# Optimization experiments

Measured on AMD Instinct MI355X. Metric: run time of the kernel, lower is better.

The kernel has to match this reference:

```python
import jax, jax.numpy as jnp
import numpy as np

EPS = 1e-30


def _logmmexp(P, logW):
    """Stable logsumexp_k(P[..., k] + logW[a, k]) -> (..., a) via max-shifted matmul."""
    mP = jnp.max(P, axis=-1, keepdims=True)          # (..., 1)
    mW = jnp.max(logW, axis=-1, keepdims=True)       # (A, 1)
    out = jnp.einsum('...k,ak->...a', jnp.exp(P - mP), jnp.exp(logW - mW))
    return jnp.log(out) + mP + mW[:, 0]


def _inside_chart(tokens, log_binary, log_lexical):
    B, L = tokens.shape
    N = log_binary.shape[0]
    chart = jnp.full((B, N, L, L + 1), -jnp.inf, dtype=log_lexical.dtype)
    # Base case: chart[:, :, i, i+1] = log_lexical[:, tokens[:, i]]
    lex = jnp.transpose(log_lexical[:, tokens], (1, 0, 2))  # (B, N, L)
    ii = jnp.arange(L)
    chart = chart.at[:, :, ii, ii + 1].set(lex)
    # CKY recursion: loop over span length (structural, static), vectorize over
    # start positions i and split points k.
    for s in range(2, L + 1):
        pos = L - s + 1
        i = np.arange(pos)
        m = np.arange(s - 1)
        k_idx = i[:, None] + m[None, :] + 1                 # (pos, s-1) split points
        left = chart[:, :, i[:, None], k_idx]               # (B, N, pos, s-1)
        right = chart[:, :, k_idx, (i + s)[:, None]]        # (B, N, pos, s-1)
        lt = jnp.transpose(left, (0, 2, 3, 1))              # (B, pos, m, N_B)
        rt = jnp.transpose(right, (0, 2, 3, 1))             # (B, pos, m, N_C)
        # P[b,i,m,B,C] = left + right
        P = lt[..., :, None] + rt[..., None, :]             # (B, pos, m, N, N)
        Pf = P.reshape(B, pos, (s - 1) * N * N)
        logW = jnp.broadcast_to(log_binary[:, None, :, :], (N, s - 1, N, N)).reshape(N, -1)
        scores = _logmmexp(Pf, logW)                        # (B, pos, N_A)
        chart = chart.at[:, :, i, i + s].set(jnp.transpose(scores, (0, 2, 1)))
    return chart


def setup_inputs() -> dict:
    key = jax.random.key(0)
    k1, k2, k3 = jax.random.split(key, 3)
    B, L, N, T = 32, 32, 48, 32000
    tokens = jax.random.randint(k1, (B, L), 0, T)
    binary = jax.random.uniform(k2, (N, N, N), dtype=jnp.float32)
    lexical = jax.random.uniform(k3, (N, T), dtype=jnp.float32)
    return {"tokens": tokens, "binary": binary, "lexical": lexical}


def reference(tokens, binary, lexical):
    start = 0
    log_binary = jnp.log(jnp.clip(binary, EPS))
    log_lexical = jnp.log(jnp.clip(lexical, EPS))
    chart = _inside_chart(tokens, log_binary, log_lexical)
    return chart[:, start, 0, tokens.shape[1]]  # (B,) sentence log-probs
```

## Files before the change

### kernel.cpp

```cpp
#include <hip/hip_runtime.h>
#include <math.h>

#define NNT 48
#define LL 32
#define BB 32
#define N2 2304
#define KSTEPS 72
#define EPSV 1e-30f
#define CH_J ((LL+1)*NNT)
#define SEB_S 2328
#define PD_RS 20
#define PD_T  328
#define PD_W  984
#define NCELL (BB*LL*(LL+1)*NNT)

typedef __attribute__((ext_vector_type(8))) short bf16x8;
typedef __attribute__((ext_vector_type(4))) float f32x4;
typedef __attribute__((ext_vector_type(4))) int   i32x4;

__device__ __forceinline__ int ch_idx(int b, int i, int j, int n) {
    return (((b*LL + i)*(LL+1) + j)*NNT + n);
}
__device__ __forceinline__ unsigned short f2bf(float x) {
    unsigned u = __float_as_uint(x);
    u = (u + 0x7fffu + ((u >> 16) & 1u)) >> 16;
    return (unsigned short)u;
}
__device__ __forceinline__ int cvtpk(float lo, float hi) {
    int r;
    asm("v_cvt_pk_bf16_f32 %0, %1, %2" : "=v"(r) : "v"(lo), "v"(hi));
    return r;
}
__device__ __forceinline__ int uvt_base(int q, int r, int kc) {
    return q*1536 + ((((r << 2) + kc) ^ (r & 7)) << 3);
}
__device__ __forceinline__ float wavemax(float x) {
    #pragma unroll
    for (int o = 32; o; o >>= 1) x = fmaxf(x, __shfl_xor(x, o));
    return x;
}
__device__ __forceinline__ float ch_ld(const float* p) {
    return __hip_atomic_load(p, __ATOMIC_RELAXED, __HIP_MEMORY_SCOPE_AGENT);
}
__device__ __forceinline__ void ch_st(float* p, float v) {
    __hip_atomic_store(p, v, __ATOMIC_RELAXED, __HIP_MEMORY_SCOPE_AGENT);
}
#define LBAR() { asm volatile("s_waitcnt lgkmcnt(0)" ::: "memory"); \
                 __builtin_amdgcn_s_barrier(); }

__global__ void prep_kernel(const float* __restrict__ binary, const int* __restrict__ tokens,
                            const float* __restrict__ lexical, unsigned short* __restrict__ Wp,
                            float* __restrict__ chart, int T) {
    if (blockIdx.x < 432) {
        int idx = blockIdx.x*256 + threadIdx.x;
        int j  = idx & 7;
        int l  = (idx >> 3) & 63;
        int ks = (idx >> 9) % KSTEPS;
        int nt = idx / (KSTEPS*512);
        int e = ks*32 + ((l >> 4) << 3) + j;
        int n = nt*16 + (l & 15);
        int bp = e % 48, c = e / 48;
        Wp[idx] = f2bf(fmaxf(binary[n*N2 + bp*48 + c], EPSV));
    } else if (blockIdx.x < 688) {
        int row = (blockIdx.x - 432)*4 + (threadIdx.x >> 6);
        int lane = threadIdx.x & 63;
        int b = row >> 5, i = row & 31;
        int tok = tokens[b*LL + i];
        float val = (lane < NNT)
            ? __logf(fmaxf(lexical[(size_t)lane*(size_t)T + (size_t)tok], EPSV))
            : -INFINITY;
        float rm = wavemax(val);
        if (lane < NNT) chart[ch_idx(b, i, i+1, lane)] = val;
        if (lane == 0) chart[ch_idx(b, i, 0, i+1)] = rm;
    } else {
        int idx = (blockIdx.x - 688)*256 + threadIdx.x;
        if (idx < NCELL) {
            int n = idx % NNT;
            int r = idx / NNT;
            int j = r % (LL + 1);
            int i = (r / (LL + 1)) % LL;
            if (j != i + 1 && !(j == 0 && n == i + 1))
                chart[idx] = -INFINITY;
        }
    }
}

#define MFMA16(A,B,C) __builtin_amdgcn_mfma_f32_16x16x32_bf16(A,B,C,0,0,0)

#define LDVP(V, C, TCX, VPX)                                                   \
    { _Pragma("unroll")                                                        \
      for (int dt = 0; dt < 8; ++dt) {                                         \
          int t = (C)*8 + dt; int tt = (t < (TCX)) ? t : (TCX) - 1;            \
          int kk = rr + tt*2;                                                  \
          V[dt] = ch_ld((VPX) + kk*CH_J + ln);                                 \
      } }
#define FRESHFIX(V)                                                            \
    { if (freshLDS) {                                                          \
          if (lane == 0) btP = sRm[q + 1][s - 1];                              \
          if (rr == 0) V[0] = sOut[q + 1][ln];                                 \
      } }
#define CONSCH(V, C)                                                           \
    { int pv[4];                                                               \
      _Pragma("unroll")                                                        \
      for (int dp = 0; dp < 4; ++dp) {                                         \
          int t0 = (C)*8 + 2*dp;                                               \
          int tt0 = (t0     < tc) ? t0     : tc - 1;                           \
          int tt1 = (t0 + 1 < tc) ? t0 + 1 : tc - 1;                           \
          float a0 = sRm[q][rr + tt0*2 + 1];                                   \
          float a1 = sRm[q][rr + tt1*2 + 1];                                   \
          float e0 = __expf(V[2*dp]     + a0 - M);                             \
          float e1 = __expf(V[2*dp + 1] + a1 - M);                             \
          pv[dp] = cvtpk(e0, e1);                                              \
      }                                                                        \
      if (lane < NNT) {                                                        \
          int ad = uvt_base(w, lane, (C));                                     \
          *(i32x4*)&sUV[12288 + ad] = (i32x4){pv[0],pv[1],pv[2],pv[3]};        \
      } }

__global__ __launch_bounds__(512, 2) void inside_kernel(
        const unsigned short* __restrict__ Wp,
        float* __restrict__ chart,
        float* __restrict__ out) {
    const int pb = blockIdx.x;
    const int b = pb & 31, c = pb >> 5;
    const int i_base = 28 - 4*c;
    const int tid = threadIdx.x, lane = tid & 63, w = tid >> 6;
    const int fr = lane & 15, kg = lane >> 4;
    const int ln = (lane < NNT) ? lane : 0;
    const int q = w >> 1, rr = w & 1;
    const int i0 = i_base + q;

    __shared__ __align__(16) short sUV[24576];
    __shared__ __align__(16) short sEb[16*SEB_S];
    __shared__ float pD[8*PD_W];
    __shared__ float sRm[4][33];
    __shared__ float sOut[4][NNT];

    for (int x = tid; x < 12288; x += 512) ((int*)sUV)[x] = 0;
    for (int x = tid; x < 18624; x += 512) ((int*)sEb)[x] = 0;
    if (tid < 4)
        sRm[tid][1] = ch_ld(&chart[ch_idx(b, i_base + tid, 0, i_base + tid + 1)]);
    if (w < 4 && lane < NNT)
        sOut[w][lane] = ch_ld(&chart[ch_idx(b, i_base + w, i_base + w + 1, lane)]);

    const bf16x8* wp8 = (const bf16x8*)Wp;
    const int kstart = 9*w;
    bf16x8 wreg[9][3];
    #pragma unroll
    for (int t = 0; t < 9; ++t)
        #pragma unroll
        for (int nt = 0; nt < 3; ++nt)
            wreg[t][nt] = wp8[(nt*KSTEPS + kstart + t)*64 + lane];

    float vvP0[8] = {0,0,0,0,0,0,0,0}, vvP1[8] = {0,0,0,0,0,0,0,0}, btP = 0.f;
    if (i0 <= LL - 2) {
        const int nkn = 1, tcn = (nkn - rr + 1) >> 1;
        if (tcn > 0) {
            const float* vpn = chart + ch_idx(b, i0 + 1, i0 + 2, 0);
            const float* bpn = chart + ch_idx(b, i0 + 1, 0, i0 + 2);
            btP = (lane < nkn) ? ch_ld(bpn + lane*CH_J) : 0.f;
            LDVP(vvP0, 0, tcn, vpn)
        }
    }

    __syncthreads();

    for (int s = 2; s <= LL; ++s) {
        const int nk = s - 1;
        if (i_base > LL - s) return;

        const bool active = (i0 <= LL - s);
        const int tc = active ? ((nk - rr + 1) >> 1) : 0;
        const bool freshLDS = active && (s > 2) && (q < 3);
        float M = -INFINITY;
        f32x4 ea[9];
        #pragma unroll
        for (int z = 0; z < 9; ++z) ea[z] = (f32x4){0.f, 0.f, 0.f, 0.f};

        if (active && rr == ((nk - 1) & 1) && lane < NNT) {
            int tn = (nk - 1 - rr) >> 1;
            float eu = __expf(sOut[q][lane] - sRm[q][s - 1]);
            sUV[uvt_base(w, lane, tn >> 3) + (tn & 7)] = (short)f2bf(eu);
        }

        if (tc > 0) {
            const float* vp = chart + ch_idx(b, i0 + 1, i0 + s, 0);
            const float* bp = chart + ch_idx(b, i0 + 1, 0, i0 + s);

            FRESHFIX(vvP0)
            for (;;) {
                bool bad = (lane < nk) && (btP == -INFINITY);
                #pragma unroll
                for (int dt = 0; dt < 8; ++dt) bad |= (vvP0[dt] == -INFINITY);
                if (tc > 8) {
                    #pragma unroll
                    for (int dt = 0; dt < 8; ++dt) bad |= (vvP1[dt] == -INFINITY);
                }
                if (!__any(bad)) break;
                btP = (lane < nk) ? ch_ld(bp + lane*CH_J) : 0.f;
                LDVP(vvP0, 0, tc, vp)
                if (tc > 8) { LDVP(vvP1, 1, tc, vp) }
                FRESHFIX(vvP0)
            }

            {
                float al = (lane < nk) ? sRm[q][lane + 1] : -INFINITY;
                M = wavemax((lane < nk) ? al + btP : -INFINITY);
            }

            CONSCH(vvP0, 0)
            if (tc > 8) { CONSCH(vvP1, 1) }

            bf16x8 A0 = *(const bf16x8*)&sUV[uvt_base(w,  0 + fr, kg)];
            bf16x8 A1 = *(const bf16x8*)&sUV[uvt_base(w, 16 + fr, kg)];
            bf16x8 A2 = *(const bf16x8*)&sUV[uvt_base(w, 32 + fr, kg)];
            bf16x8 B0 = *(const bf16x8*)&sUV[12288 + uvt_base(w,  0 + fr, kg)];
            bf16x8 B1 = *(const bf16x8*)&sUV[12288 + uvt_base(w, 16 + fr, kg)];
            bf16x8 B2 = *(const bf16x8*)&sUV[12288 + uvt_base(w, 32 + fr, kg)];
            ea[0] = MFMA16(A0,B0,ea[0]); ea[1] = MFMA16(A0,B1,ea[1]); ea[2] = MFMA16(A0,B2,ea[2]);
            ea[3] = MFMA16(A1,B0,ea[3]); ea[4] = MFMA16(A1,B1,ea[4]); ea[5] = MFMA16(A1,B2,ea[5]);
            ea[6] = MFMA16(A2,B0,ea[6]); ea[7] = MFMA16(A2,B1,ea[7]); ea[8] = MFMA16(A2,B2,ea[8]);
        }

        if (s < LL && i0 <= LL - s - 1) {
            const int nkn = s;
            const int tcn = (nkn - rr + 1) >> 1;
            const float* vpn = chart + ch_idx(b, i0 + 1, i0 + s + 1, 0);
            const float* bpn = chart + ch_idx(b, i0 + 1, 0, i0 + s + 1);
            btP = (lane < nkn) ? ch_ld(bpn + lane*CH_J) : 0.f;
            LDVP(vvP0, 0, tcn, vpn)
            if (tcn > 8) { LDVP(vvP1, 1, tcn, vpn) }
        }

        if (active) {
            #pragma unroll
            for (int mt = 0; mt < 3; ++mt) {
                #pragma unroll
                for (int ct = 0; ct < 3; ++ct) {
                    f32x4 d = ea[mt*3 + ct];
                    int e0 = (ct*16 + fr)*48 + mt*16 + kg*4;
                    unsigned lo = (unsigned)cvtpk(d[0], d[1]);
                    unsigned hi = (unsigned)cvtpk(d[2], d[3]);
                    *(unsigned long long*)&sEb[w*SEB_S + e0] =
                        (unsigned long long)lo | ((unsigned long long)hi << 32);
                }
            }
        }

        LBAR();

        {
            f32x4 c0 = {0.f,0.f,0.f,0.f}, c1 = c0, c2 = c0;
            #pragma unroll
            for (int t = 0; t < 9; ++t) {
                bf16x8 af = *(const bf16x8*)&sEb[fr*SEB_S + (kstart + t)*32 + kg*8];
                c0 = MFMA16(af, wreg[t][0], c0);
                c1 = MFMA16(af, wreg[t][1], c1);
                c2 = MFMA16(af, wreg[t][2], c2);
            }
            #pragma unroll
            for (int r2 = 0; r2 < 4; ++r2) {
                int row = kg*4 + r2;
                pD[w*PD_W + 0*PD_T + row*PD_RS + fr] = c0[r2];
                pD[w*PD_W + 1*PD_T + row*PD_RS + fr] = c1[r2];
                pD[w*PD_W + 2*PD_T + row*PD_RS + fr] = c2[r2];
            }
        }
        LBAR();

        if (active && rr == 0) {
            float sum = 0.f;
            #pragma unroll
            for (int w2 = 0; w2 < 8; ++w2) {
                const float* pp = &pD[w2*PD_W + (ln >> 4)*PD_T + (ln & 15)];
                sum += pp[(2*q)*PD_RS] + pp[(2*q + 1)*PD_RS];
            }
            float val = M + __logf(sum);
            float rm = wavemax((lane < NNT) ? val : -INFINITY);
            if (lane < NNT) {
                ch_st(&chart[ch_idx(b, i0, i0 + s, lane)], val);
                sOut[q][lane] = val;
            }
            if (lane == 0) {
                ch_st(&chart[ch_idx(b, i0, 0, i0 + s)], rm);
                sRm[q][s] = rm;
                if (s == LL) out[b] = val;
            }
        }
        LBAR();
    }
}

extern "C" void kernel_launch(void* const* d_in, const int* in_sizes, int n_in,
                              void* d_out, int out_size, void* d_ws, size_t ws_size,
                              hipStream_t stream) {
    const int*   tokens  = (const int*)d_in[0];
    const float* binary  = (const float*)d_in[1];
    const float* lexical = (const float*)d_in[2];
    float* out = (float*)d_out;

    float* chart = (float*)d_ws;
    unsigned short* Wp = (unsigned short*)(chart + (size_t)NCELL);

    int T = in_sizes[2] / NNT;

    int fill_blocks = (NCELL + 255)/256;
    prep_kernel<<<688 + fill_blocks, 256, 0, stream>>>(binary, tokens, lexical, Wp, chart, T);
    inside_kernel<<<256, 512, 0, stream>>>(Wp, chart, out);
}
```

Baseline: 127.3 us.

## Defer freshest split-point contribution into a rank-1 MFMA after main product

Each wave no longer waits for the just-computed neighbor cell (split k=i+1) before its main MFMA. It zeroes that slot, runs the bulk product, and then adds the fresh term as a separate rank-1 MFMA pass using shuffled exp values. The previous step's left-operand exp row is now written into LDS by the producing wave right after it finishes its reduction, not at the start of the next step. This shortens the serial dependency between span steps, at the cost of nine extra MFMAs, shuffles and a clamped exponent on the fresh term.

```diff
diff --git a/kernel.cpp b/kernel.cpp
--- a/kernel.cpp
+++ b/kernel.cpp
@@ -94,11 +94,6 @@
           int kk = rr + tt*2;                                                  \
           V[dt] = ch_ld((VPX) + kk*CH_J + ln);                                 \
       } }
-#define FRESHFIX(V)                                                            \
-    { if (freshLDS) {                                                          \
-          if (lane == 0) btP = sRm[q + 1][s - 1];                              \
-          if (rr == 0) V[0] = sOut[q + 1][ln];                                 \
-      } }
 #define CONSCH(V, C)                                                           \
     { int pv[4];                                                               \
       _Pragma("unroll")                                                        \
@@ -110,11 +105,12 @@
           float a1 = sRm[q][rr + tt1*2 + 1];                                   \
           float e0 = __expf(V[2*dp]     + a0 - M);                             \
           float e1 = __expf(V[2*dp + 1] + a1 - M);                             \
+          if ((C) == 0 && dp == 0 && zfix) e0 = 0.f;                           \
           pv[dp] = cvtpk(e0, e1);                                              \
       }                                                                        \
       if (lane < NNT) {                                                        \
           int ad = uvt_base(w, lane, (C));                                     \
-          *(i32x4*)&sUV[12288 + ad] = (i32x4){pv[0],pv[1],pv[2],pv[3]};        \
+          *(i32x4*)&sUV[ad + 12288] = (i32x4){pv[0],pv[1],pv[2],pv[3]};        \
       } }
 
 __global__ __launch_bounds__(512, 2) void inside_kernel(
@@ -165,33 +161,42 @@
 
     __syncthreads();
 
+    float eu0reg = (lane < NNT) ? __expf(sOut[q][lane] - sRm[q][1]) : 0.f;
+    if (rr == 0 && lane < NNT)
+        sUV[uvt_base(w, lane, 0)] = (short)f2bf(eu0reg);
+
     for (int s = 2; s <= LL; ++s) {
         const int nk = s - 1;
         if (i_base > LL - s) return;
 
         const bool active = (i0 <= LL - s);
         const int tc = active ? ((nk - rr + 1) >> 1) : 0;
-        const bool freshLDS = active && (s > 2) && (q < 3);
+        const bool defer = (s > 2);
+        const int zfix = (defer && rr == 0) ? 1 : 0;
         float M = -INFINITY;
         f32x4 ea[9];
         #pragma unroll
         for (int z = 0; z < 9; ++z) ea[z] = (f32x4){0.f, 0.f, 0.f, 0.f};
 
-        if (active && rr == ((nk - 1) & 1) && lane < NNT) {
-            int tn = (nk - 1 - rr) >> 1;
-            float eu = __expf(sOut[q][lane] - sRm[q][s - 1]);
-            sUV[uvt_base(w, lane, tn >> 3) + (tn & 7)] = (short)f2bf(eu);
-        }
-
         if (tc > 0) {
             const float* vp = chart + ch_idx(b, i0 + 1, i0 + s, 0);
             const float* bp = chart + ch_idx(b, i0 + 1, 0, i0 + s);
 
-            FRESHFIX(vvP0)
+            float vfresh = 0.f;
+            if (defer && q == 3 && rr == 0) vfresh = ch_ld(vp + ln);
+
             for (;;) {
-                bool bad = (lane < nk) && (btP == -INFINITY);
-                #pragma unroll
-                for (int dt = 0; dt < 8; ++dt) bad |= (vvP0[dt] == -INFINITY);
+                bool bad;
+                if (defer) {
+                    bad = (lane >= 1 && lane < nk) && (btP == -INFINITY);
+                    #pragma unroll
+                    for (int dt = 0; dt < 8; ++dt)
+                        if (!(rr == 0 && dt == 0)) bad |= (vvP0[dt] == -INFINITY);
+                } else {
+                    bad = (lane < nk) && (btP == -INFINITY);
+                    #pragma unroll
+                    for (int dt = 0; dt < 8; ++dt) bad |= (vvP0[dt] == -INFINITY);
+                }
                 if (tc > 8) {
                     #pragma unroll
                     for (int dt = 0; dt < 8; ++dt) bad |= (vvP1[dt] == -INFINITY);
@@ -200,12 +205,12 @@
                 btP = (lane < nk) ? ch_ld(bp + lane*CH_J) : 0.f;
                 LDVP(vvP0, 0, tc, vp)
                 if (tc > 8) { LDVP(vvP1, 1, tc, vp) }
-                FRESHFIX(vvP0)
             }
 
             {
                 float al = (lane < nk) ? sRm[q][lane + 1] : -INFINITY;
-                M = wavemax((lane < nk) ? al + btP : -INFINITY);
+                bool use = defer ? (lane >= 1 && lane < nk) : (lane < nk);
+                M = wavemax(use ? (al + btP) : -INFINITY);
             }
 
             CONSCH(vvP0, 0)
@@ -220,6 +225,36 @@
             ea[0] = MFMA16(A0,B0,ea[0]); ea[1] = MFMA16(A0,B1,ea[1]); ea[2] = MFMA16(A0,B2,ea[2]);
             ea[3] = MFMA16(A1,B0,ea[3]); ea[4] = MFMA16(A1,B1,ea[4]); ea[5] = MFMA16(A1,B2,ea[5]);
             ea[6] = MFMA16(A2,B0,ea[6]); ea[7] = MFMA16(A2,B1,ea[7]); ea[8] = MFMA16(A2,B2,ea[8]);
+
+            if (defer && rr == 0) {
+                float v0;
+                if (q < 3) {
+                    v0 = sOut[q + 1][ln];
+                } else {
+                    for (;;) {
+                        if (!__any((lane < NNT) && (vfresh == -INFINITY))) break;
+                        vfresh = ch_ld(vp + ln);
+                    }
+                    v0 = vfresh;
+                }
+                float a0s = sRm[q][1];
+                float ev0 = (lane < NNT) ? __expf(fminf(v0 + a0s - M, 80.f)) : 0.f;
+                float sA0 = __shfl(eu0reg, fr), sA1 = __shfl(eu0reg, 16 + fr),
+                      sA2 = __shfl(eu0reg, 32 + fr);
+                float sB0 = __shfl(ev0, fr), sB1 = __shfl(ev0, 16 + fr),
+                      sB2 = __shfl(ev0, 32 + fr);
+                bf16x8 z8 = {0,0,0,0,0,0,0,0};
+                bf16x8 Ar0 = z8, Ar1 = z8, Ar2 = z8, Br0 = z8, Br1 = z8, Br2 = z8;
+                if (kg == 0) {
+                    Ar0[0] = (short)f2bf(sA0); Ar1[0] = (short)f2bf(sA1);
+                    Ar2[0] = (short)f2bf(sA2);
+                    Br0[0] = (short)f2bf(sB0); Br1[0] = (short)f2bf(sB1);
+                    Br2[0] = (short)f2bf(sB2);
+                }
+                ea[0] = MFMA16(Ar0,Br0,ea[0]); ea[1] = MFMA16(Ar0,Br1,ea[1]); ea[2] = MFMA16(Ar0,Br2,ea[2]);
+                ea[3] = MFMA16(Ar1,Br0,ea[3]); ea[4] = MFMA16(Ar1,Br1,ea[4]); ea[5] = MFMA16(Ar1,Br2,ea[5]);
+                ea[6] = MFMA16(Ar2,Br0,ea[6]); ea[7] = MFMA16(Ar2,Br1,ea[7]); ea[8] = MFMA16(Ar2,Br2,ea[8]);
+            }
         }
 
         if (s < LL && i0 <= LL - s - 1) {
@@ -280,6 +315,10 @@
             if (lane < NNT) {
                 ch_st(&chart[ch_idx(b, i0, i0 + s, lane)], val);
                 sOut[q][lane] = val;
+                int rrn = (s - 1) & 1;
+                int tn  = (s - 1 - rrn) >> 1;
+                sUV[uvt_base(2*q + rrn, lane, tn >> 3) + (tn & 7)] =
+                    (short)f2bf(__expf(val - rm));
             }
             if (lane == 0) {
                 ch_st(&chart[ch_idx(b, i0, 0, i0 + s)], rm);
```

After: 125.1 us. No clear change (-1.7%).

## Remove second per-step barrier by recomputing neighbour results redundantly in registers

Applied to the files above, without the earlier changes.

All waves, not just rr==0, now reduce the partial sums after the barrier. Each wave also recomputes its neighbour row's value and row-max into registers, so the fresh left/right operands no longer go through shared memory. This lets the trailing per-span barrier and the sOut array be dropped, and the diagonal exp term is written directly by the producing wave. The cost is duplicated reduction work and a max value published through sM, which adds some hazard risk from shared memory that is no longer guarded by a barrier.

```diff
diff --git a/kernel.cpp b/kernel.cpp
--- a/kernel.cpp
+++ b/kernel.cpp
@@ -94,11 +94,6 @@
           int kk = rr + tt*2;                                                  \
           V[dt] = ch_ld((VPX) + kk*CH_J + ln);                                 \
       } }
-#define FRESHFIX(V)                                                            \
-    { if (freshLDS) {                                                          \
-          if (lane == 0) btP = sRm[q + 1][s - 1];                              \
-          if (rr == 0) V[0] = sOut[q + 1][ln];                                 \
-      } }
 #define CONSCH(V, C)                                                           \
     { int pv[4];                                                               \
       _Pragma("unroll")                                                        \
@@ -114,7 +109,7 @@
       }                                                                        \
       if (lane < NNT) {                                                        \
           int ad = uvt_base(w, lane, (C));                                     \
-          *(i32x4*)&sUV[12288 + ad] = (i32x4){pv[0],pv[1],pv[2],pv[3]};        \
+          *(i32x4*)&sUV[ad + 12288] = (i32x4){pv[0],pv[1],pv[2],pv[3]};        \
       } }
 
 __global__ __launch_bounds__(512, 2) void inside_kernel(
@@ -134,14 +129,12 @@
     __shared__ __align__(16) short sEb[16*SEB_S];
     __shared__ float pD[8*PD_W];
     __shared__ float sRm[4][33];
-    __shared__ float sOut[4][NNT];
+    __shared__ float sM[4];
 
     for (int x = tid; x < 12288; x += 512) ((int*)sUV)[x] = 0;
     for (int x = tid; x < 18624; x += 512) ((int*)sEb)[x] = 0;
     if (tid < 4)
         sRm[tid][1] = ch_ld(&chart[ch_idx(b, i_base + tid, 0, i_base + tid + 1)]);
-    if (w < 4 && lane < NNT)
-        sOut[w][lane] = ch_ld(&chart[ch_idx(b, i_base + w, i_base + w + 1, lane)]);
 
     const bf16x8* wp8 = (const bf16x8*)Wp;
     const int kstart = 9*w;
@@ -165,33 +158,48 @@
 
     __syncthreads();
 
+    {
+        float lf = ch_ld(&chart[ch_idx(b, i0, i0 + 1, ln)]);
+        float rmOwn = wavemax((lane < NNT) ? lf : -INFINITY);
+        if (rr == 0 && lane < NNT)
+            sUV[uvt_base(w, lane, 0)] = (short)f2bf(__expf(lf - rmOwn));
+    }
+
+    float v0Reg = 0.f, rmN = -INFINITY;
+
     for (int s = 2; s <= LL; ++s) {
         const int nk = s - 1;
         if (i_base > LL - s) return;
 
         const bool active = (i0 <= LL - s);
         const int tc = active ? ((nk - rr + 1) >> 1) : 0;
-        const bool freshLDS = active && (s > 2) && (q < 3);
         float M = -INFINITY;
         f32x4 ea[9];
         #pragma unroll
         for (int z = 0; z < 9; ++z) ea[z] = (f32x4){0.f, 0.f, 0.f, 0.f};
 
-        if (active && rr == ((nk - 1) & 1) && lane < NNT) {
-            int tn = (nk - 1 - rr) >> 1;
-            float eu = __expf(sOut[q][lane] - sRm[q][s - 1]);
-            sUV[uvt_base(w, lane, tn >> 3) + (tn & 7)] = (short)f2bf(eu);
-        }
-
         if (tc > 0) {
             const float* vp = chart + ch_idx(b, i0 + 1, i0 + s, 0);
             const float* bp = chart + ch_idx(b, i0 + 1, 0, i0 + s);
 
-            FRESHFIX(vvP0)
+            float vfresh = -INFINITY, b0fresh = -INFINITY;
+            if (s > 2 && q == 3) {
+                if (rr == 0) vfresh = ch_ld(vp + ln);
+                b0fresh = ch_ld(bp);
+            }
+
             for (;;) {
-                bool bad = (lane < nk) && (btP == -INFINITY);
-                #pragma unroll
-                for (int dt = 0; dt < 8; ++dt) bad |= (vvP0[dt] == -INFINITY);
+                bool bad;
+                if (s > 2) {
+                    bad = (lane >= 1 && lane < nk) && (btP == -INFINITY);
+                    #pragma unroll
+                    for (int dt = 0; dt < 8; ++dt)
+                        if (!(rr == 0 && dt == 0)) bad |= (vvP0[dt] == -INFINITY);
+                } else {
+                    bad = (lane < nk) && (btP == -INFINITY);
+                    #pragma unroll
+                    for (int dt = 0; dt < 8; ++dt) bad |= (vvP0[dt] == -INFINITY);
+                }
                 if (tc > 8) {
                     #pragma unroll
                     for (int dt = 0; dt < 8; ++dt) bad |= (vvP1[dt] == -INFINITY);
@@ -200,13 +208,26 @@
                 btP = (lane < nk) ? ch_ld(bp + lane*CH_J) : 0.f;
                 LDVP(vvP0, 0, tc, vp)
                 if (tc > 8) { LDVP(vvP1, 1, tc, vp) }
-                FRESHFIX(vvP0)
+            }
+            if (s > 2 && q == 3) {
+                for (;;) {
+                    bool bad = ((rr == 0) && (lane < NNT) && (vfresh == -INFINITY))
+                             || ((lane == 0) && (b0fresh == -INFINITY));
+                    if (!__any(bad)) break;
+                    if (rr == 0 && vfresh == -INFINITY) vfresh = ch_ld(vp + ln);
+                    if (b0fresh == -INFINITY) b0fresh = ch_ld(bp);
+                }
             }
 
             {
+                float btv = btP;
+                if (s > 2 && lane == 0) btv = (q < 3) ? rmN : b0fresh;
                 float al = (lane < nk) ? sRm[q][lane + 1] : -INFINITY;
-                M = wavemax((lane < nk) ? al + btP : -INFINITY);
-            }
+                M = wavemax((lane < nk) ? al + btv : -INFINITY);
+            }
+            if (rr == 0 && lane == 0) sM[q] = M;
+
+            if (s > 2 && rr == 0) vvP0[0] = (q < 3) ? v0Reg : vfresh;
 
             CONSCH(vvP0, 0)
             if (tc > 8) { CONSCH(vvP1, 1) }
@@ -268,26 +289,45 @@
         }
         LBAR();
 
-        if (active && rr == 0) {
+        if (active) {
+            const float Mq = sM[q];
             float sum = 0.f;
             #pragma unroll
             for (int w2 = 0; w2 < 8; ++w2) {
                 const float* pp = &pD[w2*PD_W + (ln >> 4)*PD_T + (ln & 15)];
                 sum += pp[(2*q)*PD_RS] + pp[(2*q + 1)*PD_RS];
             }
-            float val = M + __logf(sum);
+            float val = Mq + __logf(sum);
             float rm = wavemax((lane < NNT) ? val : -INFINITY);
-            if (lane < NNT) {
-                ch_st(&chart[ch_idx(b, i0, i0 + s, lane)], val);
-                sOut[q][lane] = val;
-            }
-            if (lane == 0) {
-                ch_st(&chart[ch_idx(b, i0, 0, i0 + s)], rm);
-                sRm[q][s] = rm;
-                if (s == LL) out[b] = val;
-            }
-        }
-        LBAR();
+            if (rr == 0) {
+                if (lane < NNT) ch_st(&chart[ch_idx(b, i0, i0 + s, lane)], val);
+                if (lane == 0) {
+                    ch_st(&chart[ch_idx(b, i0, 0, i0 + s)], rm);
+                    if (s == LL) out[b] = val;
+                }
+            }
+            if (lane == 0) sRm[q][s] = rm;
+            {
+                int rrn = (s - 1) & 1;
+                if (rr == rrn && lane < NNT) {
+                    int tn = (s - 1 - rrn) >> 1;
+                    sUV[uvt_base(w, lane, tn >> 3) + (tn & 7)] =
+                        (short)f2bf(__expf(val - rm));
+                }
+            }
+            if (q < 3 && (i0 + 1) <= LL - s) {
+                const float MqN = sM[q + 1];
+                float sum2 = 0.f;
+                #pragma unroll
+                for (int w2 = 0; w2 < 8; ++w2) {
+                    const float* pp = &pD[w2*PD_W + (ln >> 4)*PD_T + (ln & 15)];
+                    sum2 += pp[(2*q + 2)*PD_RS] + pp[(2*q + 3)*PD_RS];
+                }
+                float valN = MqN + __logf(sum2);
+                rmN = wavemax((lane < NNT) ? valN : -INFINITY);
+                v0Reg = valN;
+            }
+        }
     }
 }
 
```

New measurement: 123.3 us. -3.2%, faster.
